# Optimization experiments

Hardware: AMD Instinct MI355X
Metric: run time of the kernel (lower is better)

Reference implementation:

```python
import jax, jax.numpy as jnp
import numpy as np

B, S, H = 32, 4096, 1024


def setup_inputs() -> dict:
    key = jax.random.key(0)
    k1, k2 = jax.random.split(key)
    lstm_outputs = jax.random.normal(k1, (B, S, H), dtype=jnp.float32)
    w_attn = jax.random.normal(k2, (H,), dtype=jnp.float32) * (1.0 / np.sqrt(H))
    return {"lstm_outputs": lstm_outputs, "w_attn": w_attn}


def reference(lstm_outputs, w_attn):
    # energy: [B, S] = tanh(lstm_outputs @ w)
    energy = jnp.tanh(jnp.einsum("bsh,h->bs", lstm_outputs, w_attn))
    attn = jax.nn.softmax(energy, axis=1)  # softmax over sequence dim
    # context: [B, H] weighted sum over sequence
    context = jnp.einsum("bs,bsh->bh", attn, lstm_outputs)
    return context
```

## Files before the change

### kernel.cpp

```cpp
#include <hip/hip_runtime.h>
#include <math.h>

#define BB 32
#define SS 4096
#define HH 1024
#define CHUNKS 32
#define ROWS_PER_BLOCK (SS / CHUNKS)
#define WAVES 4
#define ROWS_PER_WAVE (ROWS_PER_BLOCK / WAVES)
#define UNROLL 2

__device__ __forceinline__ float softmax_w(float s) {
    float t  = __expf(2.0f * s);
    float th = 1.0f - 2.0f * __builtin_amdgcn_rcpf(t + 1.0f);
    return __expf(th);
}

__device__ __forceinline__ void load_rows(float4 (&buf)[UNROLL][4],
                                          const float* __restrict__ p) {
#pragma unroll
    for (int u = 0; u < UNROLL; ++u)
#pragma unroll
        for (int k = 0; k < 4; ++k)
            buf[u][k] = *(const float4*)(p + u * HH + k * 256);
}

__device__ __forceinline__ void process_rows(const float4 (&buf)[UNROLL][4],
                                             const float4 (&wv)[4],
                                             float4 (&acc)[4], float& l) {
    float s[UNROLL];
#pragma unroll
    for (int u = 0; u < UNROLL; ++u) {
        float t = 0.f;
#pragma unroll
        for (int k = 0; k < 4; ++k) {
            t = fmaf(buf[u][k].x, wv[k].x, t);
            t = fmaf(buf[u][k].y, wv[k].y, t);
            t = fmaf(buf[u][k].z, wv[k].z, t);
            t = fmaf(buf[u][k].w, wv[k].w, t);
        }
        s[u] = t;
    }
#pragma unroll
    for (int off = 32; off >= 1; off >>= 1)
#pragma unroll
        for (int u = 0; u < UNROLL; ++u)
            s[u] += __shfl_xor(s[u], off, 64);

#pragma unroll
    for (int u = 0; u < UNROLL; ++u) {
        float pw = softmax_w(s[u]);
        l += pw;
#pragma unroll
        for (int k = 0; k < 4; ++k) {
            acc[k].x = fmaf(pw, buf[u][k].x, acc[k].x);
            acc[k].y = fmaf(pw, buf[u][k].y, acc[k].y);
            acc[k].z = fmaf(pw, buf[u][k].z, acc[k].z);
            acc[k].w = fmaf(pw, buf[u][k].w, acc[k].w);
        }
    }
}

__global__ __launch_bounds__(256, 3) void attn_pass1(
    const float* __restrict__ x, const float* __restrict__ w,
    float* __restrict__ pc, float* __restrict__ pl)
{
    const int tid  = threadIdx.x;
    const int wave = tid >> 6;
    const int lane = tid & 63;
    const int blk  = blockIdx.x;
    const int b    = blk / CHUNKS;
    const int chunk= blk % CHUNKS;

    const float* xb = x + (long long)b * SS * HH
                        + (long long)chunk * ROWS_PER_BLOCK * HH
                        + (long long)wave * ROWS_PER_WAVE * HH
                        + lane * 4;

    float4 wv[4];
#pragma unroll
    for (int k = 0; k < 4; ++k)
        wv[k] = *(const float4*)(w + k * 256 + lane * 4);

    float4 acc[4];
#pragma unroll
    for (int k = 0; k < 4; ++k) acc[k] = make_float4(0.f, 0.f, 0.f, 0.f);
    float l = 0.f;

    float4 bufA[UNROLL][4], bufB[UNROLL][4];
    load_rows(bufA, xb);

    for (int r = 0; r < ROWS_PER_WAVE; r += 2 * UNROLL) {
        load_rows(bufB, xb + (long long)(r + UNROLL) * HH);
        process_rows(bufA, wv, acc, l);
        if (r + 2 * UNROLL < ROWS_PER_WAVE)
            load_rows(bufA, xb + (long long)(r + 2 * UNROLL) * HH);
        process_rows(bufB, wv, acc, l);
    }

    __shared__ float lds_c[WAVES * HH];
    __shared__ float lds_l[WAVES];
#pragma unroll
    for (int k = 0; k < 4; ++k)
        *(float4*)(lds_c + wave * HH + k * 256 + lane * 4) = acc[k];
    if (lane == 0) lds_l[wave] = l;
    __syncthreads();

    float4 c = *(const float4*)(lds_c + tid * 4);
#pragma unroll
    for (int wv2 = 1; wv2 < WAVES; ++wv2) {
        float4 o = *(const float4*)(lds_c + wv2 * HH + tid * 4);
        c.x += o.x; c.y += o.y; c.z += o.z; c.w += o.w;
    }
    *(float4*)(pc + (long long)blk * HH + tid * 4) = c;
    if (tid == 0)
        pl[blk] = lds_l[0] + lds_l[1] + lds_l[2] + lds_l[3];
}

__global__ __launch_bounds__(256) void attn_pass2(
    const float* __restrict__ pc, const float* __restrict__ pl,
    float* __restrict__ out)
{
    const int b = blockIdx.x;
    const int t = threadIdx.x;
    float l = 0.f;
    float4 c = make_float4(0.f, 0.f, 0.f, 0.f);
#pragma unroll
    for (int i = 0; i < CHUNKS; ++i) {
        const int blk = b * CHUNKS + i;
        l += pl[blk];
        float4 o = *(const float4*)(pc + (long long)blk * HH + t * 4);
        c.x += o.x; c.y += o.y; c.z += o.z; c.w += o.w;
    }
    const float inv = 1.f / l;
    float4 r = make_float4(c.x * inv, c.y * inv, c.z * inv, c.w * inv);
    *(float4*)(out + (long long)b * HH + t * 4) = r;
}

extern "C" void kernel_launch(void* const* d_in, const int* in_sizes, int n_in,
                              void* d_out, int out_size, void* d_ws, size_t ws_size,
                              hipStream_t stream) {
    const float* x = (const float*)d_in[0];
    const float* w = (const float*)d_in[1];
    float* out = (float*)d_out;

    float* pc = (float*)d_ws;
    float* pl = pc + (size_t)BB * CHUNKS * HH;

    attn_pass1<<<BB * CHUNKS, 256, 0, stream>>>(x, w, pc, pl);
    attn_pass2<<<BB, 256, 0, stream>>>(pc, pl, out);
}
```

Before: 675.7 us.

## Process eight rows per step with a two-phase reload instead of register double-buffering

Replaces the register double-buffered two-row pipeline with an eight-row step. It first loads the row slices to compute the dot products and softmax weights, then reloads the same rows from cache to accumulate the weighted context. This frees registers so occupancy can rise to four blocks per SIMD set, and it issues more independent loads at once. The cost is that every row is read twice, relying on L2 hits for the second read.

```diff
diff --git a/kernel.cpp b/kernel.cpp
--- a/kernel.cpp
+++ b/kernel.cpp
@@ -8,7 +8,7 @@
 #define ROWS_PER_BLOCK (SS / CHUNKS)
 #define WAVES 4
 #define ROWS_PER_WAVE (ROWS_PER_BLOCK / WAVES)
-#define UNROLL 2
+#define U 8
 
 __device__ __forceinline__ float softmax_w(float s) {
     float t  = __expf(2.0f * s);
@@ -16,52 +16,7 @@
     return __expf(th);
 }
 
-__device__ __forceinline__ void load_rows(float4 (&buf)[UNROLL][4],
-                                          const float* __restrict__ p) {
-#pragma unroll
-    for (int u = 0; u < UNROLL; ++u)
-#pragma unroll
-        for (int k = 0; k < 4; ++k)
-            buf[u][k] = *(const float4*)(p + u * HH + k * 256);
-}
-
-__device__ __forceinline__ void process_rows(const float4 (&buf)[UNROLL][4],
-                                             const float4 (&wv)[4],
-                                             float4 (&acc)[4], float& l) {
-    float s[UNROLL];
-#pragma unroll
-    for (int u = 0; u < UNROLL; ++u) {
-        float t = 0.f;
-#pragma unroll
-        for (int k = 0; k < 4; ++k) {
-            t = fmaf(buf[u][k].x, wv[k].x, t);
-            t = fmaf(buf[u][k].y, wv[k].y, t);
-            t = fmaf(buf[u][k].z, wv[k].z, t);
-            t = fmaf(buf[u][k].w, wv[k].w, t);
-        }
-        s[u] = t;
-    }
-#pragma unroll
-    for (int off = 32; off >= 1; off >>= 1)
-#pragma unroll
-        for (int u = 0; u < UNROLL; ++u)
-            s[u] += __shfl_xor(s[u], off, 64);
-
-#pragma unroll
-    for (int u = 0; u < UNROLL; ++u) {
-        float pw = softmax_w(s[u]);
-        l += pw;
-#pragma unroll
-        for (int k = 0; k < 4; ++k) {
-            acc[k].x = fmaf(pw, buf[u][k].x, acc[k].x);
-            acc[k].y = fmaf(pw, buf[u][k].y, acc[k].y);
-            acc[k].z = fmaf(pw, buf[u][k].z, acc[k].z);
-            acc[k].w = fmaf(pw, buf[u][k].w, acc[k].w);
-        }
-    }
-}
-
-__global__ __launch_bounds__(256, 3) void attn_pass1(
+__global__ __launch_bounds__(256, 4) void attn_pass1(
     const float* __restrict__ x, const float* __restrict__ w,
     float* __restrict__ pc, float* __restrict__ pl)
 {
@@ -87,15 +42,55 @@
     for (int k = 0; k < 4; ++k) acc[k] = make_float4(0.f, 0.f, 0.f, 0.f);
     float l = 0.f;
 
-    float4 bufA[UNROLL][4], bufB[UNROLL][4];
-    load_rows(bufA, xb);
+    for (int r = 0; r < ROWS_PER_WAVE; r += U) {
+        const float* xr = xb + (long long)r * HH;
 
-    for (int r = 0; r < ROWS_PER_WAVE; r += 2 * UNROLL) {
-        load_rows(bufB, xb + (long long)(r + UNROLL) * HH);
-        process_rows(bufA, wv, acc, l);
-        if (r + 2 * UNROLL < ROWS_PER_WAVE)
-            load_rows(bufA, xb + (long long)(r + 2 * UNROLL) * HH);
-        process_rows(bufB, wv, acc, l);
+        float t[U];
+#pragma unroll
+        for (int u = 0; u < U; ++u) t[u] = 0.f;
+
+#pragma unroll
+        for (int k = 0; k < 4; ++k) {
+            float4 v[U];
+#pragma unroll
+            for (int u = 0; u < U; ++u)
+                v[u] = *(const float4*)(xr + (long long)u * HH + k * 256);
+#pragma unroll
+            for (int u = 0; u < U; ++u) {
+                t[u] = fmaf(v[u].x, wv[k].x, t[u]);
+                t[u] = fmaf(v[u].y, wv[k].y, t[u]);
+                t[u] = fmaf(v[u].z, wv[k].z, t[u]);
+                t[u] = fmaf(v[u].w, wv[k].w, t[u]);
+            }
+        }
+
+#pragma unroll
+        for (int off = 32; off >= 1; off >>= 1)
+#pragma unroll
+            for (int u = 0; u < U; ++u)
+                t[u] += __shfl_xor(t[u], off, 64);
+
+        float p[U];
+#pragma unroll
+        for (int u = 0; u < U; ++u) {
+            p[u] = softmax_w(t[u]);
+            l += p[u];
+        }
+
+#pragma unroll
+        for (int k = 0; k < 4; ++k) {
+            float4 v[U];
+#pragma unroll
+            for (int u = 0; u < U; ++u)
+                v[u] = *(const float4*)(xr + (long long)u * HH + k * 256);
+#pragma unroll
+            for (int u = 0; u < U; ++u) {
+                acc[k].x = fmaf(p[u], v[u].x, acc[k].x);
+                acc[k].y = fmaf(p[u], v[u].y, acc[k].y);
+                acc[k].z = fmaf(p[u], v[u].z, acc[k].z);
+                acc[k].w = fmaf(p[u], v[u].w, acc[k].w);
+            }
+        }
     }
 
     __shared__ float lds_c[WAVES * HH];
```

After: 724.9 us. +7.3%, slower.
